# Performance work log

Measured on AMD Instinct MI355X. Metric: run time of the kernel, lower is better.

The kernel has to match this reference:

```python
import jax, jax.numpy as jnp
import numpy as np

K = 10  # neighbors (k = min(k, N-1); N=4096 >> 10)
EPS = 1e-5  # InstanceNorm eps (torch default)


def knn_idx(coords, k):
    # coords: [B,3,N] -> indices of k nearest neighbors (excluding self) [B,N,k]
    pts = coords.transpose(0, 2, 1)  # [B,N,3]
    sq = jnp.sum(pts * pts, axis=-1)  # [B,N]
    dist = sq[:, :, None] + sq[:, None, :] - 2.0 * jnp.einsum('bnc,bmc->bnm', pts, pts)
    dist = jnp.clip(dist, 1e-12)
    _, idx = jax.lax.top_k(-dist, k + 1)  # ascending distance, sorted
    return idx[:, :, 1:]  # drop self


def graph_feature(idx, feats):
    # feats: [B,C,N], idx: [B,N,k] -> [B,2C,N,k] = [center, neighbor-center]
    neigh = jax.vmap(lambda f, i: f[:, i])(feats, idx)  # [B,C,N,k]
    center = jnp.broadcast_to(feats[..., None], neigh.shape)
    return jnp.concatenate([center, neigh - center], axis=1)


def instance_norm(x):
    # x: [B,C,N,k]; normalize over spatial dims per (batch, channel), no affine
    mu = jnp.mean(x, axis=(2, 3), keepdims=True)
    var = jnp.var(x, axis=(2, 3), keepdims=True)
    return (x - mu) * jax.lax.rsqrt(var + EPS)


def lrelu(x):
    return jnp.where(x >= 0, x, 0.2 * x)


def setup_inputs() -> dict:
    key = jax.random.key(0)
    k1, k2, k3, k4, k5 = jax.random.split(key, 5)
    B, C, N = 4, 128, 4096
    coords = jax.random.normal(k1, (B, 3, N), dtype=jnp.float32)
    features = jax.random.normal(k2, (B, C, N), dtype=jnp.float32)
    W1 = jax.random.normal(k3, (C, 2 * C), dtype=jnp.float32) * 0.05
    W2 = jax.random.normal(k4, (2 * C, 2 * C), dtype=jnp.float32) * 0.05
    W3 = jax.random.normal(k5, (C, 4 * C), dtype=jnp.float32) * 0.05
    return {"coords": coords, "features": features, "W1": W1, "W2": W2, "W3": W3}


def reference(coords, features, W1, W2, W3):
    idx = knn_idx(coords, K)  # same KNN graph used by both EdgeConv stages
    x0 = features  # [B,C,N]
    # stage 1: EdgeConv C -> C
    g1 = graph_feature(idx, x0)  # [B,2C,N,k]
    x1 = lrelu(instance_norm(jnp.einsum('oc,bcnk->bonk', W1, g1)))
    x1 = jnp.max(x1, axis=-1)  # [B,C,N]
    # stage 2: EdgeConv C -> 2C
    g2 = graph_feature(idx, x1)  # [B,2C,N,k] (input C, cat -> 2C)
    x2 = lrelu(instance_norm(jnp.einsum('oc,bcnk->bonk', W2, g2)))
    x2 = jnp.max(x2, axis=-1)  # [B,2C,N]
    # fuse: [x0,x1,x2] -> 4C -> C via conv1x1 + InstanceNorm (spatial = N)
    x3 = jnp.concatenate([x0, x1, x2], axis=1)  # [B,4C,N]
    x3 = jnp.einsum('oc,bcn->bon', W3, x3)[..., None]  # [B,C,N,1]
    x3 = lrelu(instance_norm(x3))[..., 0]  # [B,C,N]
    return x3
```

## Files before the change

kernel.cpp:

```cpp
#include <hip/hip_runtime.h>
#include <math.h>
#include <stdint.h>

#define NB 4
#define NC 128
#define NP 4096
#define KNN 10


__device__ __forceinline__ uint16_t f2bf(float f) {
  uint32_t u = __float_as_uint(f);
  u += 0x7fffu + ((u >> 16) & 1u);
  return (uint16_t)(u >> 16);
}
__device__ __forceinline__ float bf2f(uint16_t h) {
  return __uint_as_float(((uint32_t)h) << 16);
}

__device__ __forceinline__ void async16(const void* g, void* l) {
  __builtin_amdgcn_global_load_lds(
      (const __attribute__((address_space(1))) unsigned int*)g,
      (__attribute__((address_space(3))) unsigned int*)l,
      16, 0, 0);
}

__device__ __forceinline__ uint32_t fsort(float f) {
  uint32_t u = __float_as_uint(f);
  return (u & 0x80000000u) ? ~u : (u | 0x80000000u);
}
__device__ __forceinline__ float funsort(uint32_t k) {
  uint32_t u = (k & 0x80000000u) ? (k & 0x7fffffffu) : ~k;
  return __uint_as_float(u);
}

typedef __bf16 bf16x8 __attribute__((ext_vector_type(8)));
typedef float f32x4 __attribute__((ext_vector_type(4)));

__global__ void k_prep(const float* __restrict__ W1, const float* __restrict__ W2,
                       const float* __restrict__ W3, const float* __restrict__ coords,
                       uint16_t* __restrict__ W1cat, uint16_t* __restrict__ W2cat,
                       uint16_t* __restrict__ W3b,
                       float* __restrict__ stats, float4* __restrict__ pts4) {
  int t = blockIdx.x * 256 + threadIdx.x;
  if (t < 32768) {
    int o = t >> 7, c = t & 127;
    float v;
    if (o < 128) v = W1[o * 256 + c] - W1[o * 256 + 128 + c];
    else         v = W1[(o - 128) * 256 + 128 + c];
    W1cat[t] = f2bf(v);
  } else if (t < 98304) {
    int t2 = t - 32768;
    int o = t2 >> 7, c = t2 & 127;
    float v;
    if (o < 256) v = W2[o * 256 + c] - W2[o * 256 + 128 + c];
    else         v = W2[(o - 256) * 256 + 128 + c];
    W2cat[t2] = f2bf(v);
  } else if (t < 163840) {
    int t2 = t - 98304;
    W3b[t2] = f2bf(W3[t2]);
  } else if (t < 163840 + 8192) {
    stats[t - 163840] = 0.f;
  } else if (t < 163840 + 8192 + 16384) {
    int t2 = t - 163840 - 8192;
    int b = t2 >> 12, n = t2 & 4095;
    const float* cb = coords + b * 12288;
    float x = cb[n], y = cb[4096 + n], z = cb[8192 + n];
    float w = fmaf(x, x, fmaf(y, y, z * z));
    pts4[t2] = make_float4(x, y, z, w);
  }
}

__global__ void k_trans_feat(const float* __restrict__ feat, uint16_t* __restrict__ Xcat) {
  __shared__ float tile[32][33];
  int bid = blockIdx.x;
  int b = bid >> 9;
  int r = bid & 511;
  int n0 = (r >> 2) << 5;
  int c0 = (r & 3) << 5;
  int tx = threadIdx.x & 31, ty = threadIdx.x >> 5;
#pragma unroll
  for (int i = 0; i < 4; i++) {
    int c = c0 + ty + i * 8;
    tile[ty + i * 8][tx] = feat[(b * 128 + c) * 4096 + n0 + tx];
  }
  __syncthreads();
#pragma unroll
  for (int i = 0; i < 4; i++) {
    int n = n0 + ty + i * 8;
    Xcat[((b * 4096 + n) * 512) + c0 + tx] = f2bf(tile[tx][ty + i * 8]);
  }
}

__global__ void k_knn_thr(const float4* __restrict__ pts4, float* __restrict__ candd) {
  int L = blockIdx.x;
  int ch = L & 7;
  int qb = (L >> 3) & 15;
  int b = L >> 7;
  int m0 = ch << 7;
  const float4* pb = pts4 + b * 4096;
  int t = threadIdx.x;
  int q = (qb << 8) + t;
  float4 qp = pb[q];
  float d10[10];
#pragma unroll
  for (int i = 0; i < 10; i++) d10[i] = 1e30f;
#pragma unroll 2
  for (int mm = 0; mm < 128; mm++) {
    int m = m0 + mm;
    float4 p = pb[m];
    float dot = fmaf(qp.x, p.x, fmaf(qp.y, p.y, qp.z * p.z));
    float s = qp.w + p.w;
    float d = fmaf(-2.f, dot, s);
    d = (m == q) ? 1e30f : d;
    if (d < d10[9]) {
      float carry = d;
#pragma unroll
      for (int i = 0; i < 10; i++) {
        float lo = fminf(d10[i], carry);
        carry = fmaxf(d10[i], carry);
        d10[i] = lo;
      }
    }
  }
  int row = b * 4096 + q;
#pragma unroll
  for (int i = 0; i < 10; i++) candd[row * 80 + ch * 10 + i] = d10[i];
}

__global__ void k_knn_merge(const float* __restrict__ candd, float* __restrict__ tq) {
  int gw = blockIdx.x * 4 + (threadIdx.x >> 6);
  int l = threadIdx.x & 63;
  const float* cp = candd + (size_t)gw * 80;
  uint32_t k0 = fsort(cp[l]);
  uint32_t k1 = (l < 16) ? fsort(cp[64 + l]) : 0xFFFFFFFFu;
  uint32_t g = 0;
#pragma unroll
  for (int it = 0; it < 10; it++) {
    uint32_t m = k0 < k1 ? k0 : k1;
#pragma unroll
    for (int s = 1; s < 64; s <<= 1) {
      uint32_t o = __shfl_xor(m, s);
      m = o < m ? o : m;
    }
    g = m;
    if (it < 9) {
      if (k0 == m) k0 = 0xFFFFFFFFu;
      else if (k1 == m) k1 = 0xFFFFFFFFu;
    }
  }
  if (l == 0) tq[gw] = funsort(g);
}

#define CFCAP 112
#define DMARGIN 1e-3f
__global__ __launch_bounds__(256) void k_knn_cf(
    const float4* __restrict__ pts4, const float* __restrict__ tq,
    int* __restrict__ idxout) {
  __shared__ int candi[8 * CFCAP];
  __shared__ int ccnt[8];
  int blk = blockIdx.x;
  int b = blk >> 9;
  int qg = blk & 511;
  int t = threadIdx.x;
  if (t < 8) ccnt[t] = 0;
  const float4* pb = pts4 + b * 4096;
  int qbase = qg * 8;
  float q2x[8], q2y[8], q2z[8], rhs[8];
#pragma unroll
  for (int j = 0; j < 8; j++) {
    float4 qp = pb[qbase + j];
    q2x[j] = -2.f * qp.x; q2y[j] = -2.f * qp.y; q2z[j] = -2.f * qp.z;
    rhs[j] = tq[b * 4096 + qbase + j] + DMARGIN - qp.w;
  }
  __syncthreads();
#pragma unroll 4
  for (int c = 0; c < 16; c++) {
    float4 p = pb[c * 256 + t];
    int m = c * 256 + t;
#pragma unroll
    for (int j = 0; j < 8; j++) {
      float tt = fmaf(q2x[j], p.x, fmaf(q2y[j], p.y, fmaf(q2z[j], p.z, p.w)));
      if (tt <= rhs[j]) {
        int pos = atomicAdd(&ccnt[j], 1);
        if (pos < CFCAP) candi[j * CFCAP + pos] = m;
      }
    }
  }
  __syncthreads();
  int w = t >> 6;
  int l = t & 63;
  for (int k = 0; k < 2; k++) {
    int qloc = w * 2 + k;
    int q2 = qbase + qloc;
    float4 qp2 = pb[q2];
    int c = ccnt[qloc]; c = c < CFCAP ? c : CFCAP;
    unsigned long long k0 = ~0ULL, k1 = ~0ULL;
#pragma unroll
    for (int u = 0; u < 2; u++) {
      int j = u * 64 + l;
      if (j < c) {
        int m = candi[qloc * CFCAP + j];
        float4 p = pb[m];
        float dot = fmaf(qp2.x, p.x, fmaf(qp2.y, p.y, qp2.z * p.z));
        float s = qp2.w + p.w;
        float d = fmaf(-2.f, dot, s);
        d = (m == q2) ? 1e30f : d;
        unsigned long long key = (((unsigned long long)fsort(d)) << 32) | (uint32_t)m;
        if (u == 0) k0 = key; else k1 = key;
      }
    }
    uint32_t keep[10];
#pragma unroll
    for (int it = 0; it < 10; it++) {
      unsigned long long m = k0 < k1 ? k0 : k1;
#pragma unroll
      for (int s = 1; s < 64; s <<= 1) {
        unsigned long long o = __shfl_xor(m, s);
        m = o < m ? o : m;
      }
      keep[it] = (uint32_t)(m & 0xffffffffu);
      if (k0 == m) k0 = ~0ULL;
      else if (k1 == m) k1 = ~0ULL;
    }
    if (l == 0) {
      int orow = b * 4096 + q2;
#pragma unroll
      for (int i = 0; i < 10; i++) idxout[orow * 10 + i] = (int)keep[i];
    }
  }
}

__global__ __launch_bounds__(256) void k_gemm_bf(
    const uint16_t* __restrict__ Xb, int ldx, int xoff,
    const uint16_t* __restrict__ Wb, int ldw,
    float* __restrict__ Y, int ldy, int K,
    uint16_t* __restrict__ Ub, uint16_t* __restrict__ Vb,
    int voff, int uld, int vld,
    float* __restrict__ T1s, float* __restrict__ T2s) {
  __shared__ __align__(16) uint8_t lds[49152];
  const int t = threadIdx.x;
  const int l = t & 63;
  const int wid = t >> 6;
  const int wr = wid & 1, wc = wid >> 1;
  const int p0 = blockIdx.x * 128;
  const int o0 = blockIdx.y * 64;

  const int rA = l >> 3;
  const int cbp = ((l & 7) ^ rA) << 4;
  const int swl = (l & 7) << 4;

  f32x4 acc[4][2];
#pragma unroll
  for (int mi = 0; mi < 4; mi++)
#pragma unroll
    for (int ni = 0; ni < 2; ni++) acc[mi][ni] = (f32x4)0.f;

  auto stage = [&](int k0, int buf) {
    const uint16_t* Xs_ = Xb + (size_t)p0 * ldx + xoff + k0;
    const uint16_t* Ws_ = Wb + (size_t)o0 * ldw + k0;
#pragma unroll
    for (int cc = 0; cc < 4; cc++) {
      int c = wid * 4 + cc;
      const uint8_t* g = (const uint8_t*)(Xs_ + (size_t)(c * 8 + rA) * ldx) + cbp;
      async16(g, &lds[buf * 16384 + c * 1024]);
    }
#pragma unroll
    for (int cc = 0; cc < 2; cc++) {
      int c = wid * 2 + cc;
      const uint8_t* g = (const uint8_t*)(Ws_ + (size_t)(c * 8 + rA) * ldw) + cbp;
      async16(g, &lds[32768 + buf * 8192 + c * 1024]);
    }
  };

  auto compute = [&](int buf) {
    const uint8_t* Ab = &lds[buf * 16384];
    const uint8_t* Bb = &lds[32768 + buf * 8192];
#pragma unroll
    for (int ks = 0; ks < 2; ks++) {
      int cb = ks * 64 + ((l >> 4) << 4);
      bf16x8 bfr[2];
#pragma unroll
      for (int ni = 0; ni < 2; ni++) {
        int n = wc * 32 + ni * 16 + (l & 15);
        bfr[ni] = *(const bf16x8*)(Bb + n * 128 + (cb ^ swl));
      }
#pragma unroll
      for (int mi = 0; mi < 4; mi++) {
        int m = wr * 64 + mi * 16 + (l & 15);
        bf16x8 afr = *(const bf16x8*)(Ab + m * 128 + (cb ^ swl));
        acc[mi][0] = __builtin_amdgcn_mfma_f32_16x16x32_bf16(afr, bfr[0], acc[mi][0], 0, 0, 0);
        acc[mi][1] = __builtin_amdgcn_mfma_f32_16x16x32_bf16(afr, bfr[1], acc[mi][1], 0, 0, 0);
      }
    }
  };

  const int nsteps = K >> 6;
  stage(0, 0);
  for (int s = 0; s < nsteps; s++) {
    __syncthreads();
    if (s + 1 < nsteps) stage((s + 1) << 6, (s + 1) & 1);
    compute(s & 1);
  }

  if (Vb != nullptr) {
    const bool isv = (o0 >= voff);
#pragma unroll
    for (int mi = 0; mi < 4; mi++)
#pragma unroll
      for (int ni = 0; ni < 2; ni++) {
        int col = o0 + wc * 32 + ni * 16 + (l & 15);
        int row0 = p0 + wr * 64 + mi * 16 + (l >> 4) * 4;
#pragma unroll
        for (int j = 0; j < 4; j++) {
          if (isv) Vb[(size_t)(row0 + j) * vld + (col - voff)] = f2bf(acc[mi][ni][j]);
          else     Ub[(size_t)(row0 + j) * uld + col] = f2bf(acc[mi][ni][j]);
        }
      }
  } else {
#pragma unroll
    for (int mi = 0; mi < 4; mi++)
#pragma unroll
      for (int ni = 0; ni < 2; ni++) {
        int col = o0 + wc * 32 + ni * 16 + (l & 15);
        int row0 = p0 + wr * 64 + mi * 16 + (l >> 4) * 4;
#pragma unroll
        for (int j = 0; j < 4; j++)
          Y[(size_t)(row0 + j) * ldy + col] = acc[mi][ni][j];
      }
    if (T1s != nullptr) {
      int b = p0 >> 12;
#pragma unroll
      for (int ni = 0; ni < 2; ni++) {
        int col = o0 + wc * 32 + ni * 16 + (l & 15);
        float a1 = 0.f, a2 = 0.f;
#pragma unroll
        for (int mi = 0; mi < 4; mi++)
#pragma unroll
          for (int j = 0; j < 4; j++) {
            float y = acc[mi][ni][j];
            a1 += y;
            a2 = fmaf(y, y, a2);
          }
        a1 += __shfl_xor(a1, 16); a2 += __shfl_xor(a2, 16);
        a1 += __shfl_xor(a1, 32); a2 += __shfl_xor(a2, 32);
        if ((l >> 4) == 0) {
          atomicAdd(&T1s[b * 128 + col], a1);
          atomicAdd(&T2s[b * 128 + col], a2);
        }
      }
    }
  }
}

template <int O>
__global__ void k_gather(const uint16_t* __restrict__ Ub,
                         const uint16_t* __restrict__ Vb,
                         const int* __restrict__ idx,
                         uint16_t* __restrict__ M,
                         float* __restrict__ T1, float* __restrict__ T2) {
  int L = blockIdx.x;
  int rx = L & 7;
  int b = rx >> 1;
  int j = ((L >> 3) << 1) + (rx & 1);
  int n0 = j << 4;
  int o = threadIdx.x;
  float a1 = 0.f, a2 = 0.f;
  for (int pi = 0; pi < 16; pi++) {
    int row = b * 4096 + n0 + pi;
    float u = bf2f(Ub[(size_t)row * O + o]);
    float s1 = 0.f, s2 = 0.f, vmax = -1e30f;
#pragma unroll
    for (int jj = 0; jj < KNN; jj++) {
      int m = idx[row * 10 + jj];
      float v = bf2f(Vb[(size_t)(b * 4096 + m) * O + o]);
      s1 += v;
      float x = u + v;
      s2 = fmaf(x, x, s2);
      vmax = fmaxf(vmax, v);
    }
    M[(size_t)row * O + o] = f2bf(vmax);
    a1 += 10.f * u + s1;
    a2 += s2;
  }
  atomicAdd(&T1[b * O + o], a1);
  atomicAdd(&T2[b * O + o], a2);
}

template <int O>
__global__ void k_passB(const uint16_t* __restrict__ Ub,
                        const uint16_t* __restrict__ M, int coff,
                        const float* __restrict__ T1, const float* __restrict__ T2,
                        uint16_t* __restrict__ Xcat) {
  int t = blockIdx.x * 256 + threadIdx.x;
  int o = t & (O - 1);
  int pn = t / O;
  int b = pn >> 12;
  float mu = T1[b * O + o] * (1.f / 40960.f);
  float e2 = T2[b * O + o] * (1.f / 40960.f);
  float inv = rsqrtf(e2 - mu * mu + 1e-5f);
  float x = (bf2f(Ub[(size_t)pn * O + o]) + bf2f(M[(size_t)pn * O + o]) - mu) * inv;
  Xcat[pn * 512 + coff + o] = f2bf(x >= 0.f ? x : 0.2f * x);
}

__global__ void k_out(const float* __restrict__ Y3, const float* __restrict__ T1,
                      const float* __restrict__ T2, float* __restrict__ out) {
  __shared__ float tile[32][33];
  int bid = blockIdx.x;
  int b = bid >> 9;
  int r = bid & 511;
  int n0 = (r >> 2) << 5;
  int o0 = (r & 3) << 5;
  int tx = threadIdx.x & 31, ty = threadIdx.x >> 5;
  int o = o0 + tx;
  float mu = T1[b * 128 + o] * (1.f / 4096.f);
  float e2 = T2[b * 128 + o] * (1.f / 4096.f);
  float inv = rsqrtf(e2 - mu * mu + 1e-5f);
#pragma unroll
  for (int i = 0; i < 4; i++) {
    int n = n0 + ty + i * 8;
    float v = (Y3[(b * 4096 + n) * 128 + o] - mu) * inv;
    tile[ty + i * 8][tx] = v >= 0.f ? v : 0.2f * v;
  }
  __syncthreads();
#pragma unroll
  for (int i = 0; i < 4; i++) {
    int oo = o0 + ty + i * 8;
    out[(b * 128 + oo) * 4096 + n0 + tx] = tile[tx][ty + i * 8];
  }
}

extern "C" void kernel_launch(void* const* d_in, const int* in_sizes, int n_in,
                              void* d_out, int out_size, void* d_ws, size_t ws_size,
                              hipStream_t stream) {
  const float* coords   = (const float*)d_in[0];
  const float* features = (const float*)d_in[1];
  const float* W1       = (const float*)d_in[2];
  const float* W2       = (const float*)d_in[3];
  const float* W3       = (const float*)d_in[4];
  float* out = (float*)d_out;

  float*    ws    = (float*)d_ws;
  uint16_t* Xcat  = (uint16_t*)ws;
  float*    candd = ws + 4194304;
  float*    tq    = ws + 5505024;
  float4*   pts4  = (float4*)(ws + 5521408);
  uint16_t* Ub1   = (uint16_t*)(ws + 5586944);
  uint16_t* Ub2   = (uint16_t*)(ws + 6635520);
  uint16_t* Mbuf  = (uint16_t*)(ws + 12582912);
  float*    Y3    = ws + 14680064;
  int*      idxb  = (int*)(ws + 16777216);
  uint16_t* W1cat = (uint16_t*)(ws + 16941056);
  uint16_t* W2cat = (uint16_t*)(ws + 16957440);
  uint16_t* W3b   = (uint16_t*)(ws + 16990208);
  float*    stats = ws + 17022976;
  uint16_t* Vb1   = (uint16_t*)(ws + 17031168);
  uint16_t* Vb2   = (uint16_t*)(ws + 18079744);

  k_prep<<<736, 256, 0, stream>>>(W1, W2, W3, coords, W1cat, W2cat, W3b, stats, pts4);
  k_trans_feat<<<2048, 256, 0, stream>>>(features, Xcat);
  k_knn_thr<<<512, 256, 0, stream>>>(pts4, candd);
  k_knn_merge<<<4096, 256, 0, stream>>>(candd, tq);
  k_knn_cf<<<2048, 256, 0, stream>>>(pts4, tq, idxb);

  k_gemm_bf<<<dim3(128, 4), 256, 0, stream>>>(Xcat, 512, 0, W1cat, 128,
                                              nullptr, 0, 128,
                                              Ub1, Vb1, 128, 128, 128,
                                              nullptr, nullptr);
  k_gather<128><<<1024, 128, 0, stream>>>(Ub1, Vb1, idxb, Mbuf, stats + 0, stats + 512);
  k_passB<128><<<8192, 256, 0, stream>>>(Ub1, Mbuf, 128, stats + 0, stats + 512, Xcat);

  k_gemm_bf<<<dim3(128, 8), 256, 0, stream>>>(Xcat, 512, 128, W2cat, 128,
                                              nullptr, 0, 128,
                                              Ub2, Vb2, 256, 256, 256,
                                              nullptr, nullptr);
  k_gather<256><<<1024, 256, 0, stream>>>(Ub2, Vb2, idxb, Mbuf, stats + 1024, stats + 2048);
  k_passB<256><<<16384, 256, 0, stream>>>(Ub2, Mbuf, 256, stats + 1024, stats + 2048, Xcat);

  k_gemm_bf<<<dim3(128, 2), 256, 0, stream>>>(Xcat, 512, 0, W3b, 512,
                                              Y3, 128, 512,
                                              nullptr, nullptr, 0, 0, 0,
                                              stats + 3072, stats + 3584);
  k_out<<<2048, 256, 0, stream>>>(Y3, stats + 3072, stats + 3584, out);
}
```

Before: 160.7 us.

## Add smaller-tile GEMM for fuse stage and fold center add into gather

The final 512->128 fuse GEMM moves to a dedicated kernel with 64x64 tiles, which doubles the grid from 256 to 512 blocks so more CUs have work. The gather kernel now stores u+max(v) directly, so passB reads one bf16 buffer instead of two. The cost is extra rounding: u+vmax is now rounded to bf16 once as a sum, where before u and vmax were each rounded separately. The smaller tiles also give less operand reuse per block.

```diff
diff --git a/kernel.cpp b/kernel.cpp
--- a/kernel.cpp
+++ b/kernel.cpp
@@ -232,11 +232,9 @@
 
 __global__ __launch_bounds__(256) void k_gemm_bf(
     const uint16_t* __restrict__ Xb, int ldx, int xoff,
-    const uint16_t* __restrict__ Wb, int ldw,
-    float* __restrict__ Y, int ldy, int K,
+    const uint16_t* __restrict__ Wb, int ldw, int K,
     uint16_t* __restrict__ Ub, uint16_t* __restrict__ Vb,
-    int voff, int uld, int vld,
-    float* __restrict__ T1s, float* __restrict__ T2s) {
+    int voff, int uld, int vld) {
   __shared__ __align__(16) uint8_t lds[49152];
   const int t = threadIdx.x;
   const int l = t & 63;
@@ -302,53 +300,106 @@
     compute(s & 1);
   }
 
-  if (Vb != nullptr) {
-    const bool isv = (o0 >= voff);
-#pragma unroll
-    for (int mi = 0; mi < 4; mi++)
-#pragma unroll
-      for (int ni = 0; ni < 2; ni++) {
-        int col = o0 + wc * 32 + ni * 16 + (l & 15);
-        int row0 = p0 + wr * 64 + mi * 16 + (l >> 4) * 4;
-#pragma unroll
-        for (int j = 0; j < 4; j++) {
-          if (isv) Vb[(size_t)(row0 + j) * vld + (col - voff)] = f2bf(acc[mi][ni][j]);
-          else     Ub[(size_t)(row0 + j) * uld + col] = f2bf(acc[mi][ni][j]);
-        }
-      }
-  } else {
-#pragma unroll
-    for (int mi = 0; mi < 4; mi++)
-#pragma unroll
-      for (int ni = 0; ni < 2; ni++) {
-        int col = o0 + wc * 32 + ni * 16 + (l & 15);
-        int row0 = p0 + wr * 64 + mi * 16 + (l >> 4) * 4;
-#pragma unroll
-        for (int j = 0; j < 4; j++)
-          Y[(size_t)(row0 + j) * ldy + col] = acc[mi][ni][j];
-      }
-    if (T1s != nullptr) {
-      int b = p0 >> 12;
-#pragma unroll
-      for (int ni = 0; ni < 2; ni++) {
-        int col = o0 + wc * 32 + ni * 16 + (l & 15);
-        float a1 = 0.f, a2 = 0.f;
-#pragma unroll
-        for (int mi = 0; mi < 4; mi++)
-#pragma unroll
-          for (int j = 0; j < 4; j++) {
-            float y = acc[mi][ni][j];
-            a1 += y;
-            a2 = fmaf(y, y, a2);
-          }
-        a1 += __shfl_xor(a1, 16); a2 += __shfl_xor(a2, 16);
-        a1 += __shfl_xor(a1, 32); a2 += __shfl_xor(a2, 32);
-        if ((l >> 4) == 0) {
-          atomicAdd(&T1s[b * 128 + col], a1);
-          atomicAdd(&T2s[b * 128 + col], a2);
-        }
-      }
-    }
+  const bool isv = (o0 >= voff);
+#pragma unroll
+  for (int mi = 0; mi < 4; mi++)
+#pragma unroll
+    for (int ni = 0; ni < 2; ni++) {
+      int col = o0 + wc * 32 + ni * 16 + (l & 15);
+      int row0 = p0 + wr * 64 + mi * 16 + (l >> 4) * 4;
+#pragma unroll
+      for (int j = 0; j < 4; j++) {
+        if (isv) Vb[(size_t)(row0 + j) * vld + (col - voff)] = f2bf(acc[mi][ni][j]);
+        else     Ub[(size_t)(row0 + j) * uld + col] = f2bf(acc[mi][ni][j]);
+      }
+    }
+}
+
+__global__ __launch_bounds__(256) void k_gemm3(
+    const uint16_t* __restrict__ Xb, int ldx,
+    const uint16_t* __restrict__ Wb, int ldw,
+    float* __restrict__ Y, int ldy, int K,
+    float* __restrict__ T1s, float* __restrict__ T2s) {
+  __shared__ __align__(16) uint8_t lds[32768];
+  const int t = threadIdx.x;
+  const int l = t & 63;
+  const int wid = t >> 6;
+  const int p0 = blockIdx.x * 64;
+  const int o0 = blockIdx.y * 64;
+
+  const int rA = l >> 3;
+  const int cbp = ((l & 7) ^ rA) << 4;
+  const int swl = (l & 7) << 4;
+
+  f32x4 acc[4];
+#pragma unroll
+  for (int mi = 0; mi < 4; mi++) acc[mi] = (f32x4)0.f;
+
+  auto stage = [&](int k0, int buf) {
+    const uint16_t* Xs_ = Xb + (size_t)p0 * ldx + k0;
+    const uint16_t* Ws_ = Wb + (size_t)o0 * ldw + k0;
+#pragma unroll
+    for (int cc = 0; cc < 2; cc++) {
+      int c = wid * 2 + cc;
+      const uint8_t* g = (const uint8_t*)(Xs_ + (size_t)(c * 8 + rA) * ldx) + cbp;
+      async16(g, &lds[buf * 16384 + c * 1024]);
+    }
+#pragma unroll
+    for (int cc = 0; cc < 2; cc++) {
+      int c = wid * 2 + cc;
+      const uint8_t* g = (const uint8_t*)(Ws_ + (size_t)(c * 8 + rA) * ldw) + cbp;
+      async16(g, &lds[buf * 16384 + 8192 + c * 1024]);
+    }
+  };
+
+  auto compute = [&](int buf) {
+    const uint8_t* Ab = &lds[buf * 16384];
+    const uint8_t* Bb = &lds[buf * 16384 + 8192];
+#pragma unroll
+    for (int ks = 0; ks < 2; ks++) {
+      int cb = ks * 64 + ((l >> 4) << 4);
+      int n = wid * 16 + (l & 15);
+      bf16x8 bfr = *(const bf16x8*)(Bb + n * 128 + (cb ^ swl));
+#pragma unroll
+      for (int mi = 0; mi < 4; mi++) {
+        int m = mi * 16 + (l & 15);
+        bf16x8 afr = *(const bf16x8*)(Ab + m * 128 + (cb ^ swl));
+        acc[mi] = __builtin_amdgcn_mfma_f32_16x16x32_bf16(afr, bfr, acc[mi], 0, 0, 0);
+      }
+    }
+  };
+
+  const int nsteps = K >> 6;
+  stage(0, 0);
+  for (int s = 0; s < nsteps; s++) {
+    __syncthreads();
+    if (s + 1 < nsteps) stage((s + 1) << 6, (s + 1) & 1);
+    compute(s & 1);
+  }
+
+  int col = o0 + wid * 16 + (l & 15);
+#pragma unroll
+  for (int mi = 0; mi < 4; mi++) {
+    int row0 = p0 + mi * 16 + (l >> 4) * 4;
+#pragma unroll
+    for (int j = 0; j < 4; j++)
+      Y[(size_t)(row0 + j) * ldy + col] = acc[mi][j];
+  }
+  int b = p0 >> 12;
+  float a1 = 0.f, a2 = 0.f;
+#pragma unroll
+  for (int mi = 0; mi < 4; mi++)
+#pragma unroll
+    for (int j = 0; j < 4; j++) {
+      float y = acc[mi][j];
+      a1 += y;
+      a2 = fmaf(y, y, a2);
+    }
+  a1 += __shfl_xor(a1, 16); a2 += __shfl_xor(a2, 16);
+  a1 += __shfl_xor(a1, 32); a2 += __shfl_xor(a2, 32);
+  if ((l >> 4) == 0) {
+    atomicAdd(&T1s[b * 128 + col], a1);
+    atomicAdd(&T2s[b * 128 + col], a2);
   }
 }
 
@@ -356,7 +407,7 @@
 __global__ void k_gather(const uint16_t* __restrict__ Ub,
                          const uint16_t* __restrict__ Vb,
                          const int* __restrict__ idx,
-                         uint16_t* __restrict__ M,
+                         uint16_t* __restrict__ S,
                          float* __restrict__ T1, float* __restrict__ T2) {
   int L = blockIdx.x;
   int rx = L & 7;
@@ -378,7 +429,7 @@
       s2 = fmaf(x, x, s2);
       vmax = fmaxf(vmax, v);
     }
-    M[(size_t)row * O + o] = f2bf(vmax);
+    S[(size_t)row * O + o] = f2bf(u + vmax);
     a1 += 10.f * u + s1;
     a2 += s2;
   }
@@ -387,8 +438,7 @@
 }
 
 template <int O>
-__global__ void k_passB(const uint16_t* __restrict__ Ub,
-                        const uint16_t* __restrict__ M, int coff,
+__global__ void k_passB(const uint16_t* __restrict__ S, int coff,
                         const float* __restrict__ T1, const float* __restrict__ T2,
                         uint16_t* __restrict__ Xcat) {
   int t = blockIdx.x * 256 + threadIdx.x;
@@ -398,7 +448,7 @@
   float mu = T1[b * O + o] * (1.f / 40960.f);
   float e2 = T2[b * O + o] * (1.f / 40960.f);
   float inv = rsqrtf(e2 - mu * mu + 1e-5f);
-  float x = (bf2f(Ub[(size_t)pn * O + o]) + bf2f(M[(size_t)pn * O + o]) - mu) * inv;
+  float x = (bf2f(S[(size_t)pn * O + o]) - mu) * inv;
   Xcat[pn * 512 + coff + o] = f2bf(x >= 0.f ? x : 0.2f * x);
 }
 
@@ -446,7 +496,7 @@
   float4*   pts4  = (float4*)(ws + 5521408);
   uint16_t* Ub1   = (uint16_t*)(ws + 5586944);
   uint16_t* Ub2   = (uint16_t*)(ws + 6635520);
-  uint16_t* Mbuf  = (uint16_t*)(ws + 12582912);
+  uint16_t* Sbuf  = (uint16_t*)(ws + 12582912);
   float*    Y3    = ws + 14680064;
   int*      idxb  = (int*)(ws + 16777216);
   uint16_t* W1cat = (uint16_t*)(ws + 16941056);
@@ -462,23 +512,17 @@
   k_knn_merge<<<4096, 256, 0, stream>>>(candd, tq);
   k_knn_cf<<<2048, 256, 0, stream>>>(pts4, tq, idxb);
 
-  k_gemm_bf<<<dim3(128, 4), 256, 0, stream>>>(Xcat, 512, 0, W1cat, 128,
-                                              nullptr, 0, 128,
-                                              Ub1, Vb1, 128, 128, 128,
-                                              nullptr, nullptr);
-  k_gather<128><<<1024, 128, 0, stream>>>(Ub1, Vb1, idxb, Mbuf, stats + 0, stats + 512);
-  k_passB<128><<<8192, 256, 0, stream>>>(Ub1, Mbuf, 128, stats + 0, stats + 512, Xcat);
-
-  k_gemm_bf<<<dim3(128, 8), 256, 0, stream>>>(Xcat, 512, 128, W2cat, 128,
-                                              nullptr, 0, 128,
-                                              Ub2, Vb2, 256, 256, 256,
-                                              nullptr, nullptr);
-  k_gather<256><<<1024, 256, 0, stream>>>(Ub2, Vb2, idxb, Mbuf, stats + 1024, stats + 2048);
-  k_passB<256><<<16384, 256, 0, stream>>>(Ub2, Mbuf, 256, stats + 1024, stats + 2048, Xcat);
-
-  k_gemm_bf<<<dim3(128, 2), 256, 0, stream>>>(Xcat, 512, 0, W3b, 512,
-                                              Y3, 128, 512,
-                                              nullptr, nullptr, 0, 0, 0,
-                                              stats + 3072, stats + 3584);
+  k_gemm_bf<<<dim3(128, 4), 256, 0, stream>>>(Xcat, 512, 0, W1cat, 128, 128,
+                                              Ub1, Vb1, 128, 128, 128);
+  k_gather<128><<<1024, 128, 0, stream>>>(Ub1, Vb1, idxb, Sbuf, stats + 0, stats + 512);
+  k_passB<128><<<8192, 256, 0, stream>>>(Sbuf, 128, stats + 0, stats + 512, Xcat);
+
+  k_gemm_bf<<<dim3(128, 8), 256, 0, stream>>>(Xcat, 512, 128, W2cat, 128, 128,
+                                              Ub2, Vb2, 256, 256, 256);
+  k_gather<256><<<1024, 256, 0, stream>>>(Ub2, Vb2, idxb, Sbuf, stats + 1024, stats + 2048);
+  k_passB<256><<<16384, 256, 0, stream>>>(Sbuf, 256, stats + 1024, stats + 2048, Xcat);
+
+  k_gemm3<<<dim3(256, 2), 256, 0, stream>>>(Xcat, 512, W3b, 512, Y3, 128, 512,
+                                            stats + 3072, stats + 3584);
   k_out<<<2048, 256, 0, stream>>>(Y3, stats + 3072, stats + 3584, out);
 }
```

Result: no change. 159.1 us (-1.0%).
